# Performance work log

Hardware: AMD Instinct MI355X
Metric: run time of the kernel (lower is better)

## Reference

```python
import jax, jax.numpy as jnp
import numpy as np

DIM = 768
NUM_HEADS = 12
HEAD_DIM = DIM // NUM_HEADS
SCALE = HEAD_DIM ** -0.5
NEG = -9e15


def setup_inputs() -> dict:
    key = jax.random.key(0)
    ks = jax.random.split(key, 8)
    B, N, M, C = 4, 1024, 2048, DIM
    q = jax.random.normal(ks[0], (B, N, C), dtype=jnp.float32)
    kv = jax.random.normal(ks[1], (B, M, C), dtype=jnp.float32)
    mask = jax.random.randint(ks[2], (B, 1, N, M), 0, 2, dtype=jnp.int32)
    s = 1.0 / np.sqrt(C)
    Wq = jax.random.normal(ks[3], (C, C), dtype=jnp.float32) * s      # nn.Linear(dim, dim), no bias
    Wkv = jax.random.normal(ks[4], (2 * C, C), dtype=jnp.float32) * s  # nn.Linear(dim, 2*dim), no bias
    Wproj = jax.random.normal(ks[5], (C, C), dtype=jnp.float32) * s
    bproj = jax.random.normal(ks[6], (C,), dtype=jnp.float32) * s
    return {"q": q, "kv": kv, "Wq": Wq, "Wkv": Wkv, "Wproj": Wproj, "bproj": bproj, "mask": mask}


def reference(q, kv, Wq, Wkv, Wproj, bproj, mask):
    B, M, C = kv.shape
    _, N, _ = q.shape
    H, d = NUM_HEADS, HEAD_DIM
    # kv projection -> [B, M, 2, H, d] -> k, v: [B, H, M, d]
    kvp = (kv @ Wkv.T).reshape(B, M, 2, H, d)
    k = kvp[:, :, 0].transpose(0, 2, 1, 3)
    v = kvp[:, :, 1].transpose(0, 2, 1, 3)
    # q projection -> [B, H, N, d], pre-scaled
    qp = (q @ Wq.T).reshape(B, N, H, d).transpose(0, 2, 1, 3) * SCALE
    attn = jnp.einsum('bhnd,bhmd->bhnm', qp, k)  # [B, H, N, M]
    attn = jnp.where(mask == 0, NEG, attn)
    attn = jax.nn.softmax(attn, axis=-1)
    # attn_drop / proj_drop have rate 0.0 (eval): identity
    x = jnp.einsum('bhnm,bhmd->bhnd', attn, v)
    x = x.transpose(0, 2, 1, 3).reshape(B, N, C)
    x = x @ Wproj.T + bproj
    return x
```

## Files before the change

### kernel.cpp

```cpp
#include <hip/hip_runtime.h>
#include <hip/hip_bf16.h>


typedef short  s16x8  __attribute__((ext_vector_type(8)));
typedef short  s16x4  __attribute__((ext_vector_type(4)));
typedef __bf16 bf16x8 __attribute__((ext_vector_type(8)));
typedef float  f32x4  __attribute__((ext_vector_type(4)));

#define NUM_H 12
#define DIM   768
#define BB    4
#define NQ    1024
#define MK    2048
#define QK_SCALE_LOG2E 0.18033688f

__device__ __forceinline__ short f2b(float v) {
    __hip_bfloat16 h = __float2bfloat16(v);
    return __builtin_bit_cast(short, h);
}

__device__ __forceinline__ f32x4 mfma16(bf16x8 a, bf16x8 b, f32x4 c) {
    return __builtin_amdgcn_mfma_f32_16x16x32_bf16(a, b, c, 0, 0, 0);
}

__global__ __launch_bounds__(256) void cast_f2b_kernel(
    const float* __restrict__ s, short* __restrict__ d, int n)
{
    int i = (blockIdx.x * 256 + threadIdx.x) * 8;
    if (i >= n) return;
    float4 a = *(const float4*)(s + i);
    float4 b = *(const float4*)(s + i + 4);
    s16x8 r;
    r[0] = f2b(a.x); r[1] = f2b(a.y); r[2] = f2b(a.z); r[3] = f2b(a.w);
    r[4] = f2b(b.x); r[5] = f2b(b.y); r[6] = f2b(b.z); r[7] = f2b(b.w);
    *(s16x8*)(d + i) = r;
}

__global__ __launch_bounds__(256) void pack_mask_kernel(
    const int* __restrict__ m, unsigned* __restrict__ mb)
{
    int i = blockIdx.x * 256 + threadIdx.x;
    unsigned long long bal = __ballot(m[i] != 0);
    if ((threadIdx.x & 63) == 0) {
        int wi = i >> 5;
        mb[wi]     = (unsigned)bal;
        mb[wi + 1] = (unsigned)(bal >> 32);
    }
}

__global__ __launch_bounds__(256) void gemm_bt_kernel(
    const short* __restrict__ A, const short* __restrict__ Bt,
    int Ncols, int mode, const float* __restrict__ bias,
    short* __restrict__ outb, short* __restrict__ outb2,
    float* __restrict__ outf)
{
    __shared__ short smem[18432];
    short (*As)[72] = (short(*)[72])smem;
    short (*Bs)[72] = (short(*)[72])(smem + 9216);

    int ntiles = Ncols >> 7;
    int m0 = (blockIdx.x / ntiles) << 7;
    int n0 = (blockIdx.x % ntiles) << 7;
    int t = threadIdx.x;
    int w = t >> 6, lane = t & 63, quad = lane >> 4, l16 = lane & 15;
    int wm = (w & 1) << 6, wn = (w >> 1) << 6;

    f32x4 zero4 = {0.f, 0.f, 0.f, 0.f};
    f32x4 acc[4][4];
    for (int i = 0; i < 4; i++)
        for (int j = 0; j < 4; j++) acc[i][j] = zero4;

    int lr = t >> 1;
    int lc = (t & 1) << 5;
    const short* Ap = A + (long)(m0 + lr) * DIM + lc;
    const short* Bp = Bt + (long)(n0 + lr) * DIM + lc;

    s16x8 a8[4], b8[4];
    #pragma unroll
    for (int c = 0; c < 4; c++) {
        a8[c] = *(const s16x8*)(Ap + c * 8);
        b8[c] = *(const s16x8*)(Bp + c * 8);
    }

    for (int kt = 0; kt < DIM; kt += 64) {
        __syncthreads();
        #pragma unroll
        for (int c = 0; c < 4; c++) {
            *(s16x8*)&As[lr][lc + c * 8] = a8[c];
            *(s16x8*)&Bs[lr][lc + c * 8] = b8[c];
        }
        __syncthreads();
        if (kt + 64 < DIM) {
            #pragma unroll
            for (int c = 0; c < 4; c++) {
                a8[c] = *(const s16x8*)(Ap + kt + 64 + c * 8);
                b8[c] = *(const s16x8*)(Bp + kt + 64 + c * 8);
            }
        }
        #pragma unroll
        for (int kh = 0; kh < 2; kh++) {
            bf16x8 af[4], bfr[4];
            #pragma unroll
            for (int i = 0; i < 4; i++) {
                s16x8 tmp = *(const s16x8*)&As[wm + i * 16 + l16][kh * 32 + quad * 8];
                af[i] = __builtin_bit_cast(bf16x8, tmp);
            }
            #pragma unroll
            for (int j = 0; j < 4; j++) {
                s16x8 tmp = *(const s16x8*)&Bs[wn + j * 16 + l16][kh * 32 + quad * 8];
                bfr[j] = __builtin_bit_cast(bf16x8, tmp);
            }
            #pragma unroll
            for (int i = 0; i < 4; i++)
                #pragma unroll
                for (int j = 0; j < 4; j++)
                    acc[i][j] = mfma16(af[i], bfr[j], acc[i][j]);
        }
    }

    __syncthreads();

    if (mode == 2) {
        #pragma unroll
        for (int i = 0; i < 4; i++)
            #pragma unroll
            for (int j = 0; j < 4; j++)
                #pragma unroll
                for (int r = 0; r < 4; r++) {
                    int row = m0 + wm + i * 16 + quad * 4 + r;
                    int col = n0 + wn + j * 16 + l16;
                    outf[(long)row * DIM + col] = acc[i][j][r] + bias[col];
                }
        return;
    }

    short (*Cs)[136] = (short(*)[136])smem;
    bool vreg = (mode == 1) && (n0 >= DIM);

    if (!vreg) {
        float sc = (mode == 0) ? QK_SCALE_LOG2E : 1.0f;
        #pragma unroll
        for (int i = 0; i < 4; i++)
            #pragma unroll
            for (int j = 0; j < 4; j++)
                #pragma unroll
                for (int r = 0; r < 4; r++)
                    Cs[wm + i * 16 + quad * 4 + r][wn + j * 16 + l16] =
                        f2b(acc[i][j][r] * sc);
    } else {
        #pragma unroll
        for (int i = 0; i < 4; i++)
            #pragma unroll
            for (int j = 0; j < 4; j++) {
                int c = wn + j * 16 + l16;
                int r0 = wm + i * 16 + quad * 4;
                s16x4 pk;
                pk[0] = f2b(acc[i][j][0]); pk[1] = f2b(acc[i][j][1]);
                pk[2] = f2b(acc[i][j][2]); pk[3] = f2b(acc[i][j][3]);
                *(s16x4*)&Cs[c][r0] = pk;
            }
    }
    __syncthreads();

    if (!vreg) {
        int hb2 = n0 >> 6;
        long rowsN = (mode == 0) ? NQ : MK;
        int b = (int)(m0 / rowsN);
        int rb = (int)(m0 % rowsN);
        short* ob0 = outb + ((long)(b * NUM_H + hb2) * rowsN + rb) * 64;
        short* ob1 = outb + ((long)(b * NUM_H + hb2 + 1) * rowsN + rb) * 64;
        #pragma unroll
        for (int k2 = 0; k2 < 8; k2++) {
            int ch = k2 * 256 + t;
            int half = ch >> 10, off = ch & 1023;
            s16x8 vd = *(const s16x8*)&Cs[off >> 3][(half << 6) + ((off & 7) << 3)];
            *(s16x8*)((half ? ob1 : ob0) + off * 8) = vd;
        }
    } else {
        int hb2 = (n0 - DIM) >> 6;
        int b = m0 >> 11, rb = m0 & 2047;
        #pragma unroll
        for (int k2 = 0; k2 < 8; k2++) {
            int ch = k2 * 256 + t;
            int c = ch >> 4, woff = (ch & 15) << 3;
            s16x8 vd = *(const s16x8*)&Cs[c][woff];
            int half = c >> 6, dd = c & 63;
            *(s16x8*)(outb2 + (((long)(b * NUM_H + hb2 + half) * 64 + dd) * MK + rb) + woff) = vd;
        }
    }
}

__global__ __launch_bounds__(256) void attn_kernel(
    const short* __restrict__ qp, const short* __restrict__ kk,
    const short* __restrict__ vt, const unsigned* __restrict__ mb,
    short* __restrict__ xb)
{
    __shared__ short qs[64][72];
    __shared__ short ks[64][72];
    __shared__ short vs[64][72];
    __shared__ short ps[4][16][72];
    __shared__ unsigned mw[64][2];

    int bid = blockIdx.x;
    int nt = bid & 15;
    int bh = bid >> 4;
    int h = bh % NUM_H, b = bh / NUM_H;
    int n0 = nt << 6;
    int t = threadIdx.x, w = t >> 6, lane = t & 63, quad = lane >> 4, l16 = lane & 15;

    const short* qbase = qp + ((long)bh * NQ + n0) * 64;
    const short* kbase = kk + (long)bh * MK * 64;
    const short* vbase = vt + (long)bh * 64 * MK;
    const unsigned* mbase = mb + ((long)b * NQ + n0) * 64;

    {
        int qr = t >> 2, c0 = (t & 3) << 4;
        *(s16x8*)&qs[qr][c0]     = *(const s16x8*)(qbase + qr * 64 + c0);
        *(s16x8*)&qs[qr][c0 + 8] = *(const s16x8*)(qbase + qr * 64 + c0 + 8);
    }
    __syncthreads();
    bf16x8 aq[2];
    {
        s16x8 t0 = *(const s16x8*)&qs[(w << 4) + l16][quad * 8];
        s16x8 t1 = *(const s16x8*)&qs[(w << 4) + l16][32 + quad * 8];
        aq[0] = __builtin_bit_cast(bf16x8, t0);
        aq[1] = __builtin_bit_cast(bf16x8, t1);
    }

    int sr = t >> 2, c0 = (t & 3) << 4;
    const short* kp = kbase + (long)sr * 64 + c0;
    const short* vp = vbase + (long)sr * MK + c0;

    s16x8 k0 = *(const s16x8*)(kp);
    s16x8 k1 = *(const s16x8*)(kp + 8);
    s16x8 v0 = *(const s16x8*)(vp);
    s16x8 v1 = *(const s16x8*)(vp + 8);
    unsigned mword = (t < 128) ? mbase[(t >> 1) * 64 + (t & 1)] : 0u;

    f32x4 zero4 = {0.f, 0.f, 0.f, 0.f};
    f32x4 o[4], ol = zero4;
    for (int j = 0; j < 4; j++) o[j] = zero4;

    s16x8 ones8 = {0x3F80, 0x3F80, 0x3F80, 0x3F80, 0x3F80, 0x3F80, 0x3F80, 0x3F80};
    bf16x8 ones = __builtin_bit_cast(bf16x8, ones8);

    for (int mt = 0; mt < MK; mt += 64) {
        __syncthreads();
        *(s16x8*)&ks[sr][c0]     = k0;
        *(s16x8*)&ks[sr][c0 + 8] = k1;
        *(s16x8*)&vs[sr][c0]     = v0;
        *(s16x8*)&vs[sr][c0 + 8] = v1;
        if (t < 128) mw[t >> 1][t & 1] = mword;
        __syncthreads();
        if (mt + 64 < MK) {
            k0 = *(const s16x8*)(kp + (long)(mt + 64) * 64);
            k1 = *(const s16x8*)(kp + (long)(mt + 64) * 64 + 8);
            v0 = *(const s16x8*)(vp + mt + 64);
            v1 = *(const s16x8*)(vp + mt + 64 + 8);
            if (t < 128) mword = mbase[(t >> 1) * 64 + ((mt + 64) >> 5) + (t & 1)];
        }

        f32x4 s[4];
        for (int j = 0; j < 4; j++) s[j] = zero4;
        #pragma unroll
        for (int kh = 0; kh < 2; kh++)
            #pragma unroll
            for (int j = 0; j < 4; j++) {
                s16x8 tk = *(const s16x8*)&ks[j * 16 + l16][kh * 32 + quad * 8];
                s[j] = mfma16(aq[kh], __builtin_bit_cast(bf16x8, tk), s[j]);
            }

        #pragma unroll
        for (int rr = 0; rr < 4; rr++) {
            int qrow = (w << 4) + quad * 4 + rr;
            unsigned w0 = mw[qrow][0], w1 = mw[qrow][1];
            float e0 = __builtin_amdgcn_exp2f(s[0][rr]);
            float e1 = __builtin_amdgcn_exp2f(s[1][rr]);
            float e2 = __builtin_amdgcn_exp2f(s[2][rr]);
            float e3 = __builtin_amdgcn_exp2f(s[3][rr]);
            short p0 = ((w0 >> l16) & 1)        ? f2b(e0) : (short)0;
            short p1 = ((w0 >> (16 + l16)) & 1) ? f2b(e1) : (short)0;
            short p2 = ((w1 >> l16) & 1)        ? f2b(e2) : (short)0;
            short p3 = ((w1 >> (16 + l16)) & 1) ? f2b(e3) : (short)0;
            ps[w][quad * 4 + rr][l16]      = p0;
            ps[w][quad * 4 + rr][16 + l16] = p1;
            ps[w][quad * 4 + rr][32 + l16] = p2;
            ps[w][quad * 4 + rr][48 + l16] = p3;
        }

        #pragma unroll
        for (int kh = 0; kh < 2; kh++) {
            s16x8 tp = *(const s16x8*)&ps[w][l16][kh * 32 + quad * 8];
            bf16x8 ap = __builtin_bit_cast(bf16x8, tp);
            ol = mfma16(ap, ones, ol);
            #pragma unroll
            for (int jd = 0; jd < 4; jd++) {
                s16x8 tv = *(const s16x8*)&vs[jd * 16 + l16][kh * 32 + quad * 8];
                o[jd] = mfma16(ap, __builtin_bit_cast(bf16x8, tv), o[jd]);
            }
        }
    }

    float linv[4];
    #pragma unroll
    for (int rr = 0; rr < 4; rr++) linv[rr] = 1.0f / ol[rr];
    #pragma unroll
    for (int jd = 0; jd < 4; jd++)
        #pragma unroll
        for (int rr = 0; rr < 4; rr++)
            ps[w][quad * 4 + rr][jd * 16 + l16] = f2b(o[jd][rr] * linv[rr]);

    #pragma unroll
    for (int k2 = 0; k2 < 2; k2++) {
        int row = (lane >> 3) + k2 * 8;
        int cc = (lane & 7) << 3;
        s16x8 vd = *(const s16x8*)&ps[w][row][cc];
        *(s16x8*)(xb + ((long)b * NQ + n0 + (w << 4) + row) * DIM + h * 64 + cc) = vd;
    }
}

extern "C" void kernel_launch(void* const* d_in, const int* in_sizes, int n_in,
                              void* d_out, int out_size, void* d_ws, size_t ws_size,
                              hipStream_t stream)
{
    const float* q     = (const float*)d_in[0];
    const float* kv    = (const float*)d_in[1];
    const float* Wq    = (const float*)d_in[2];
    const float* Wkv   = (const float*)d_in[3];
    const float* Wproj = (const float*)d_in[4];
    const float* bproj = (const float*)d_in[5];
    const int*   mask  = (const int*)d_in[6];
    float* out = (float*)d_out;

    char* ws = (char*)d_ws;
    short* q_bf   = (short*)ws; ws += (size_t)4096 * 768 * 2;
    short* kv_bf  = (short*)ws; ws += (size_t)8192 * 768 * 2;
    short* Wq_bf  = (short*)ws; ws += (size_t)768 * 768 * 2;
    short* Wkv_bf = (short*)ws; ws += (size_t)1536 * 768 * 2;
    short* Wp_bf  = (short*)ws; ws += (size_t)768 * 768 * 2;
    short* qp     = (short*)ws; ws += (size_t)4096 * 768 * 2;
    short* kk     = (short*)ws; ws += (size_t)8192 * 768 * 2;
    short* vt     = (short*)ws; ws += (size_t)8192 * 768 * 2;
    short* xb     = (short*)ws; ws += (size_t)4096 * 768 * 2;
    unsigned* mbits = (unsigned*)ws;

    cast_f2b_kernel<<<1536, 256, 0, stream>>>(q, q_bf, 4096 * 768);
    cast_f2b_kernel<<<3072, 256, 0, stream>>>(kv, kv_bf, 8192 * 768);
    cast_f2b_kernel<<<288, 256, 0, stream>>>(Wq, Wq_bf, 768 * 768);
    cast_f2b_kernel<<<576, 256, 0, stream>>>(Wkv, Wkv_bf, 1536 * 768);
    cast_f2b_kernel<<<288, 256, 0, stream>>>(Wproj, Wp_bf, 768 * 768);
    pack_mask_kernel<<<32768, 256, 0, stream>>>(mask, mbits);

    gemm_bt_kernel<<<(4096 / 128) * (768 / 128), 256, 0, stream>>>(
        q_bf, Wq_bf, 768, 0, nullptr, qp, nullptr, nullptr);
    gemm_bt_kernel<<<(8192 / 128) * (1536 / 128), 256, 0, stream>>>(
        kv_bf, Wkv_bf, 1536, 1, nullptr, kk, vt, nullptr);
    attn_kernel<<<BB * NUM_H * (NQ / 64), 256, 0, stream>>>(qp, kk, vt, mbits, xb);
    gemm_bt_kernel<<<(4096 / 128) * (768 / 128), 256, 0, stream>>>(
        xb, Wp_bf, 768, 2, bproj, nullptr, nullptr, out);
}
```

Measured before the change: 256.8 us.

## Merge prep kernels, fuse QKV GEMMs, keep attention P in registers via transposed MFMA

Combines the five casts and the mask packing into one prep kernel, and runs the Q and KV projections in one launch. The attention kernel computes S transposed so each lane holds probabilities directly in the A-operand layout of f16 16x16x16 MFMAs. This removes the LDS round-trip for P and for the mask words. V is now stored as fp16 instead of bf16 to match, and the block order interleaves heads across tiles. The risks are fp16 range and precision for V and P, plus the cost of twice as many MFMA instructions in the PV product.

```diff
diff --git a/kernel.cpp b/kernel.cpp
--- a/kernel.cpp
+++ b/kernel.cpp
@@ -2,14 +2,15 @@
 #include <hip/hip_bf16.h>
 
 
-typedef short  s16x8  __attribute__((ext_vector_type(8)));
-typedef short  s16x4  __attribute__((ext_vector_type(4)));
-typedef __bf16 bf16x8 __attribute__((ext_vector_type(8)));
-typedef float  f32x4  __attribute__((ext_vector_type(4)));
+typedef short    s16x8  __attribute__((ext_vector_type(8)));
+typedef short    s16x4  __attribute__((ext_vector_type(4)));
+typedef __bf16   bf16x8 __attribute__((ext_vector_type(8)));
+typedef float    f32x4  __attribute__((ext_vector_type(4)));
+typedef _Float16 f16x4  __attribute__((ext_vector_type(4)));
+typedef _Float16 f16x2  __attribute__((ext_vector_type(2)));
 
 #define NUM_H 12
 #define DIM   768
-#define BB    4
 #define NQ    1024
 #define MK    2048
 #define QK_SCALE_LOG2E 0.18033688f
@@ -18,49 +19,68 @@
     __hip_bfloat16 h = __float2bfloat16(v);
     return __builtin_bit_cast(short, h);
 }
-
-__device__ __forceinline__ f32x4 mfma16(bf16x8 a, bf16x8 b, f32x4 c) {
+__device__ __forceinline__ short f2h(float v) {
+    _Float16 h = (_Float16)v;
+    return __builtin_bit_cast(short, h);
+}
+__device__ __forceinline__ f32x4 mfma_bf16_k32(bf16x8 a, bf16x8 b, f32x4 c) {
     return __builtin_amdgcn_mfma_f32_16x16x32_bf16(a, b, c, 0, 0, 0);
 }
-
-__global__ __launch_bounds__(256) void cast_f2b_kernel(
-    const float* __restrict__ s, short* __restrict__ d, int n)
-{
-    int i = (blockIdx.x * 256 + threadIdx.x) * 8;
-    if (i >= n) return;
-    float4 a = *(const float4*)(s + i);
-    float4 b = *(const float4*)(s + i + 4);
-    s16x8 r;
-    r[0] = f2b(a.x); r[1] = f2b(a.y); r[2] = f2b(a.z); r[3] = f2b(a.w);
-    r[4] = f2b(b.x); r[5] = f2b(b.y); r[6] = f2b(b.z); r[7] = f2b(b.w);
-    *(s16x8*)(d + i) = r;
-}
-
-__global__ __launch_bounds__(256) void pack_mask_kernel(
-    const int* __restrict__ m, unsigned* __restrict__ mb)
-{
-    int i = blockIdx.x * 256 + threadIdx.x;
-    unsigned long long bal = __ballot(m[i] != 0);
-    if ((threadIdx.x & 63) == 0) {
-        int wi = i >> 5;
-        mb[wi]     = (unsigned)bal;
-        mb[wi + 1] = (unsigned)(bal >> 32);
-    }
-}
-
-__global__ __launch_bounds__(256) void gemm_bt_kernel(
+__device__ __forceinline__ f32x4 mfma_f16_k16(f16x4 a, f16x4 b, f32x4 c) {
+    return __builtin_amdgcn_mfma_f32_16x16x16f16(a, b, c, 0, 0, 0);
+}
+__device__ __forceinline__ f16x2 pk2h(float a, float b) {
+    return __builtin_bit_cast(f16x2, __builtin_amdgcn_cvt_pkrtz(a, b));
+}
+
+__global__ __launch_bounds__(256) void prep_kernel(
+    const float* __restrict__ q, const float* __restrict__ kv,
+    const float* __restrict__ Wq, const float* __restrict__ Wkv,
+    const float* __restrict__ Wp, const int* __restrict__ mask,
+    short* __restrict__ q_bf, short* __restrict__ kv_bf,
+    short* __restrict__ Wq_bf, short* __restrict__ Wkv_bf,
+    short* __restrict__ Wp_bf, unsigned char* __restrict__ mbytes)
+{
+    int bid = blockIdx.x;
+    if (bid < 5760) {
+        const float* s; short* d; long base;
+        if (bid < 1536)      { s = q;   d = q_bf;   base = (long)bid * 2048; }
+        else if (bid < 4608) { s = kv;  d = kv_bf;  base = (long)(bid - 1536) * 2048; }
+        else if (bid < 4896) { s = Wq;  d = Wq_bf;  base = (long)(bid - 4608) * 2048; }
+        else if (bid < 5472) { s = Wkv; d = Wkv_bf; base = (long)(bid - 4896) * 2048; }
+        else                 { s = Wp;  d = Wp_bf;  base = (long)(bid - 5472) * 2048; }
+        long i = base + threadIdx.x * 8;
+        float4 a = *(const float4*)(s + i);
+        float4 b = *(const float4*)(s + i + 4);
+        s16x8 r;
+        r[0] = f2b(a.x); r[1] = f2b(a.y); r[2] = f2b(a.z); r[3] = f2b(a.w);
+        r[4] = f2b(b.x); r[5] = f2b(b.y); r[6] = f2b(b.z); r[7] = f2b(b.w);
+        *(s16x8*)(d + i) = r;
+    } else {
+        long base = (long)(bid - 5760) * 2048 + threadIdx.x * 8;
+        int4 m0 = *(const int4*)(mask + base);
+        int4 m1 = *(const int4*)(mask + base + 4);
+        unsigned v = (unsigned)(m0.x != 0)        | ((unsigned)(m0.y != 0) << 1)
+                   | ((unsigned)(m0.z != 0) << 2) | ((unsigned)(m0.w != 0) << 3)
+                   | ((unsigned)(m1.x != 0) << 4) | ((unsigned)(m1.y != 0) << 5)
+                   | ((unsigned)(m1.z != 0) << 6) | ((unsigned)(m1.w != 0) << 7);
+        mbytes[base >> 3] = (unsigned char)v;
+    }
+}
+
+__device__ __forceinline__ void gemm_core(
+    short* smem,
     const short* __restrict__ A, const short* __restrict__ Bt,
     int Ncols, int mode, const float* __restrict__ bias,
     short* __restrict__ outb, short* __restrict__ outb2,
-    float* __restrict__ outf)
-{
-    __shared__ short smem[18432];
+    float* __restrict__ outf, int bid)
+{
     short (*As)[72] = (short(*)[72])smem;
     short (*Bs)[72] = (short(*)[72])(smem + 9216);
 
     int ntiles = Ncols >> 7;
-    int m0 = (blockIdx.x / ntiles) << 7;
-    int n0 = (blockIdx.x % ntiles) << 7;
+    int m0 = (bid / ntiles) << 7;
+    int n0 = (bid % ntiles) << 7;
     int t = threadIdx.x;
     int w = t >> 6, lane = t & 63, quad = lane >> 4, l16 = lane & 15;
     int wm = (w & 1) << 6, wn = (w >> 1) << 6;
@@ -114,7 +134,7 @@
             for (int i = 0; i < 4; i++)
                 #pragma unroll
                 for (int j = 0; j < 4; j++)
-                    acc[i][j] = mfma16(af[i], bfr[j], acc[i][j]);
+                    acc[i][j] = mfma_bf16_k32(af[i], bfr[j], acc[i][j]);
         }
     }
 
@@ -155,8 +175,8 @@
                 int c = wn + j * 16 + l16;
                 int r0 = wm + i * 16 + quad * 4;
                 s16x4 pk;
-                pk[0] = f2b(acc[i][j][0]); pk[1] = f2b(acc[i][j][1]);
-                pk[2] = f2b(acc[i][j][2]); pk[3] = f2b(acc[i][j][3]);
+                pk[0] = f2h(acc[i][j][0]); pk[1] = f2h(acc[i][j][1]);
+                pk[2] = f2h(acc[i][j][2]); pk[3] = f2h(acc[i][j][3]);
                 *(s16x4*)&Cs[c][r0] = pk;
             }
     }
@@ -190,6 +210,26 @@
     }
 }
 
+__global__ __launch_bounds__(256) void gemm12_kernel(
+    const short* __restrict__ qbf, const short* __restrict__ Wqbf,
+    const short* __restrict__ kvbf, const short* __restrict__ Wkvbf,
+    short* __restrict__ qp, short* __restrict__ kk, short* __restrict__ vt)
+{
+    __shared__ short smem[18432];
+    if (blockIdx.x < 192)
+        gemm_core(smem, qbf, Wqbf, 768, 0, nullptr, qp, nullptr, nullptr, blockIdx.x);
+    else
+        gemm_core(smem, kvbf, Wkvbf, 1536, 1, nullptr, kk, vt, nullptr, blockIdx.x - 192);
+}
+
+__global__ __launch_bounds__(256) void gemm3_kernel(
+    const short* __restrict__ xb, const short* __restrict__ Wpbf,
+    const float* __restrict__ bias, float* __restrict__ out)
+{
+    __shared__ short smem[18432];
+    gemm_core(smem, xb, Wpbf, 768, 2, bias, nullptr, nullptr, out, blockIdx.x);
+}
+
 __global__ __launch_bounds__(256) void attn_kernel(
     const short* __restrict__ qp, const short* __restrict__ kk,
     const short* __restrict__ vt, const unsigned* __restrict__ mb,
@@ -198,12 +238,10 @@
     __shared__ short qs[64][72];
     __shared__ short ks[64][72];
     __shared__ short vs[64][72];
-    __shared__ short ps[4][16][72];
-    __shared__ unsigned mw[64][2];
 
     int bid = blockIdx.x;
-    int nt = bid & 15;
-    int bh = bid >> 4;
+    int bh = bid % 48;
+    int nt = bid / 48;
     int h = bh % NUM_H, b = bh / NUM_H;
     int n0 = nt << 6;
     int t = threadIdx.x, w = t >> 6, lane = t & 63, quad = lane >> 4, l16 = lane & 15;
@@ -211,7 +249,7 @@
     const short* qbase = qp + ((long)bh * NQ + n0) * 64;
     const short* kbase = kk + (long)bh * MK * 64;
     const short* vbase = vt + (long)bh * 64 * MK;
-    const unsigned* mbase = mb + ((long)b * NQ + n0) * 64;
+    const unsigned* mrow = mb + ((long)b * NQ + n0 + (w << 4) + l16) * 64;
 
     {
         int qr = t >> 2, c0 = (t & 3) << 4;
@@ -219,12 +257,12 @@
         *(s16x8*)&qs[qr][c0 + 8] = *(const s16x8*)(qbase + qr * 64 + c0 + 8);
     }
     __syncthreads();
-    bf16x8 aq[2];
+    bf16x8 bq[2];
     {
         s16x8 t0 = *(const s16x8*)&qs[(w << 4) + l16][quad * 8];
         s16x8 t1 = *(const s16x8*)&qs[(w << 4) + l16][32 + quad * 8];
-        aq[0] = __builtin_bit_cast(bf16x8, t0);
-        aq[1] = __builtin_bit_cast(bf16x8, t1);
+        bq[0] = __builtin_bit_cast(bf16x8, t0);
+        bq[1] = __builtin_bit_cast(bf16x8, t1);
     }
 
     int sr = t >> 2, c0 = (t & 3) << 4;
@@ -235,14 +273,12 @@
     s16x8 k1 = *(const s16x8*)(kp + 8);
     s16x8 v0 = *(const s16x8*)(vp);
     s16x8 v1 = *(const s16x8*)(vp + 8);
-    unsigned mword = (t < 128) ? mbase[(t >> 1) * 64 + (t & 1)] : 0u;
+    uint2 mwv = *(const uint2*)(mrow);
 
     f32x4 zero4 = {0.f, 0.f, 0.f, 0.f};
     f32x4 o[4], ol = zero4;
     for (int j = 0; j < 4; j++) o[j] = zero4;
-
-    s16x8 ones8 = {0x3F80, 0x3F80, 0x3F80, 0x3F80, 0x3F80, 0x3F80, 0x3F80, 0x3F80};
-    bf16x8 ones = __builtin_bit_cast(bf16x8, ones8);
+    const f16x4 ones = {(_Float16)1.f, (_Float16)1.f, (_Float16)1.f, (_Float16)1.f};
 
     for (int mt = 0; mt < MK; mt += 64) {
         __syncthreads();
@@ -250,14 +286,14 @@
         *(s16x8*)&ks[sr][c0 + 8] = k1;
         *(s16x8*)&vs[sr][c0]     = v0;
         *(s16x8*)&vs[sr][c0 + 8] = v1;
-        if (t < 128) mw[t >> 1][t & 1] = mword;
+        unsigned cm0 = mwv.x, cm1 = mwv.y;
         __syncthreads();
         if (mt + 64 < MK) {
             k0 = *(const s16x8*)(kp + (long)(mt + 64) * 64);
             k1 = *(const s16x8*)(kp + (long)(mt + 64) * 64 + 8);
             v0 = *(const s16x8*)(vp + mt + 64);
             v1 = *(const s16x8*)(vp + mt + 64 + 8);
-            if (t < 128) mword = mbase[(t >> 1) * 64 + ((mt + 64) >> 5) + (t & 1)];
+            mwv = *(const uint2*)(mrow + ((mt + 64) >> 5));
         }
 
         f32x4 s[4];
@@ -267,36 +303,30 @@
             #pragma unroll
             for (int j = 0; j < 4; j++) {
                 s16x8 tk = *(const s16x8*)&ks[j * 16 + l16][kh * 32 + quad * 8];
-                s[j] = mfma16(aq[kh], __builtin_bit_cast(bf16x8, tk), s[j]);
-            }
-
-        #pragma unroll
-        for (int rr = 0; rr < 4; rr++) {
-            int qrow = (w << 4) + quad * 4 + rr;
-            unsigned w0 = mw[qrow][0], w1 = mw[qrow][1];
-            float e0 = __builtin_amdgcn_exp2f(s[0][rr]);
-            float e1 = __builtin_amdgcn_exp2f(s[1][rr]);
-            float e2 = __builtin_amdgcn_exp2f(s[2][rr]);
-            float e3 = __builtin_amdgcn_exp2f(s[3][rr]);
-            short p0 = ((w0 >> l16) & 1)        ? f2b(e0) : (short)0;
-            short p1 = ((w0 >> (16 + l16)) & 1) ? f2b(e1) : (short)0;
-            short p2 = ((w1 >> l16) & 1)        ? f2b(e2) : (short)0;
-            short p3 = ((w1 >> (16 + l16)) & 1) ? f2b(e3) : (short)0;
-            ps[w][quad * 4 + rr][l16]      = p0;
-            ps[w][quad * 4 + rr][16 + l16] = p1;
-            ps[w][quad * 4 + rr][32 + l16] = p2;
-            ps[w][quad * 4 + rr][48 + l16] = p3;
-        }
-
-        #pragma unroll
-        for (int kh = 0; kh < 2; kh++) {
-            s16x8 tp = *(const s16x8*)&ps[w][l16][kh * 32 + quad * 8];
-            bf16x8 ap = __builtin_bit_cast(bf16x8, tp);
-            ol = mfma16(ap, ones, ol);
+                s[j] = mfma_bf16_k32(__builtin_bit_cast(bf16x8, tk), bq[kh], s[j]);
+            }
+
+        f16x4 pa[4];
+        #pragma unroll
+        for (int j = 0; j < 4; j++) {
+            unsigned wsel = (j < 2) ? cm0 : cm1;
+            unsigned bits = wsel >> (((j & 1) << 4) + (quad << 2));
+            float p0 = (bits & 1u)        ? __builtin_amdgcn_exp2f(s[j][0]) : 0.f;
+            float p1 = ((bits >> 1) & 1u) ? __builtin_amdgcn_exp2f(s[j][1]) : 0.f;
+            float p2 = ((bits >> 2) & 1u) ? __builtin_amdgcn_exp2f(s[j][2]) : 0.f;
+            float p3 = ((bits >> 3) & 1u) ? __builtin_amdgcn_exp2f(s[j][3]) : 0.f;
+            f16x2 lo = pk2h(p0, p1);
+            f16x2 hi = pk2h(p2, p3);
+            pa[j] = __builtin_shufflevector(lo, hi, 0, 1, 2, 3);
+        }
+
+        #pragma unroll
+        for (int j = 0; j < 4; j++) {
+            ol = mfma_f16_k16(pa[j], ones, ol);
             #pragma unroll
             for (int jd = 0; jd < 4; jd++) {
-                s16x8 tv = *(const s16x8*)&vs[jd * 16 + l16][kh * 32 + quad * 8];
-                o[jd] = mfma16(ap, __builtin_bit_cast(bf16x8, tv), o[jd]);
+                f16x4 bv = *(const f16x4*)&vs[jd * 16 + l16][j * 16 + quad * 4];
+                o[jd] = mfma_f16_k16(pa[j], bv, o[jd]);
             }
         }
     }
@@ -304,17 +334,18 @@
     float linv[4];
     #pragma unroll
     for (int rr = 0; rr < 4; rr++) linv[rr] = 1.0f / ol[rr];
+    short (*ps)[72] = (short(*)[72])&qs[w << 4];
     #pragma unroll
     for (int jd = 0; jd < 4; jd++)
         #pragma unroll
         for (int rr = 0; rr < 4; rr++)
-            ps[w][quad * 4 + rr][jd * 16 + l16] = f2b(o[jd][rr] * linv[rr]);
+            ps[quad * 4 + rr][jd * 16 + l16] = f2b(o[jd][rr] * linv[rr]);
 
     #pragma unroll
     for (int k2 = 0; k2 < 2; k2++) {
         int row = (lane >> 3) + k2 * 8;
         int cc = (lane & 7) << 3;
-        s16x8 vd = *(const s16x8*)&ps[w][row][cc];
+        s16x8 vd = *(const s16x8*)&ps[row][cc];
         *(s16x8*)(xb + ((long)b * NQ + n0 + (w << 4) + row) * DIM + h * 64 + cc) = vd;
     }
 }
@@ -342,20 +373,11 @@
     short* kk     = (short*)ws; ws += (size_t)8192 * 768 * 2;
     short* vt     = (short*)ws; ws += (size_t)8192 * 768 * 2;
     short* xb     = (short*)ws; ws += (size_t)4096 * 768 * 2;
-    unsigned* mbits = (unsigned*)ws;
-
-    cast_f2b_kernel<<<1536, 256, 0, stream>>>(q, q_bf, 4096 * 768);
-    cast_f2b_kernel<<<3072, 256, 0, stream>>>(kv, kv_bf, 8192 * 768);
-    cast_f2b_kernel<<<288, 256, 0, stream>>>(Wq, Wq_bf, 768 * 768);
-    cast_f2b_kernel<<<576, 256, 0, stream>>>(Wkv, Wkv_bf, 1536 * 768);
-    cast_f2b_kernel<<<288, 256, 0, stream>>>(Wproj, Wp_bf, 768 * 768);
-    pack_mask_kernel<<<32768, 256, 0, stream>>>(mask, mbits);
-
-    gemm_bt_kernel<<<(4096 / 128) * (768 / 128), 256, 0, stream>>>(
-        q_bf, Wq_bf, 768, 0, nullptr, qp, nullptr, nullptr);
-    gemm_bt_kernel<<<(8192 / 128) * (1536 / 128), 256, 0, stream>>>(
-        kv_bf, Wkv_bf, 1536, 1, nullptr, kk, vt, nullptr);
-    attn_kernel<<<BB * NUM_H * (NQ / 64), 256, 0, stream>>>(qp, kk, vt, mbits, xb);
-    gemm_bt_kernel<<<(4096 / 128) * (768 / 128), 256, 0, stream>>>(
-        xb, Wp_bf, 768, 2, bproj, nullptr, nullptr, out);
-}
+    unsigned char* mbytes = (unsigned char*)ws;
+
+    prep_kernel<<<9856, 256, 0, stream>>>(q, kv, Wq, Wkv, Wproj, mask,
+                                          q_bf, kv_bf, Wq_bf, Wkv_bf, Wp_bf, mbytes);
+    gemm12_kernel<<<960, 256, 0, stream>>>(q_bf, Wq_bf, kv_bf, Wkv_bf, qp, kk, vt);
+    attn_kernel<<<768, 256, 0, stream>>>(qp, kk, vt, (const unsigned*)mbytes, xb);
+    gemm3_kernel<<<192, 256, 0, stream>>>(xb, Wp_bf, bproj, out);
+}
```

Result: faster. 221.7 us (-13.7%).
